# Performance work log

Hardware: AMD Instinct MI355X
Metric: run time of the kernel (lower is better)

The kernel has to match this reference:

```python
import jax, jax.numpy as jnp
import numpy as np

# Keyed conv layer as structured SpMM in affine coordinates.
# W (N x N sparse, N = C*H*W + 1) stored in ELL format: for each output row r,
# cols[r, :] are the K column indices and vals[r, :] the nonzero values.
C, H, W_, KS = 32, 32, 32, 3
N = C * H * W_ + 1          # 32769, homogeneous (+1 bias) dim
K = C * KS * KS             # 288 nnz per row (Toeplitz conv structure)
B = 32                      # batch


def setup_inputs() -> dict:
    key = jax.random.key(0)
    k1, k2, k3 = jax.random.split(key, 3)
    x_affine = jax.random.normal(k1, (B, N), dtype=jnp.float32)
    cols = jax.random.randint(k2, (N, K), 0, N, dtype=jnp.int32)
    vals = jax.random.normal(k3, (N, K), dtype=jnp.float32) / np.float32(np.sqrt(K))
    return {"x_affine": x_affine, "vals": vals, "cols": cols}


def reference(x_affine, vals, cols):
    # y = (W @ x_affine^T)^T  with W in row-wise ELL format.
    # Gather input features addressed by each row's nonzero columns, then
    # contract over the K nonzeros of each row.
    xg = x_affine[:, cols]                      # [B, N, K] gathered features
    y = jnp.einsum('bnk,nk->bn', xg, vals)      # [B, N]
    return y
```

## Files before the change

### kernel.cpp

```cpp
#include <hip/hip_runtime.h>

constexpr int B = 32;
constexpr int N = 32 * 32 * 32 + 1;
constexpr int K = 32 * 3 * 3;

using i4 = __attribute__((ext_vector_type(4))) int;
using f4 = __attribute__((ext_vector_type(4))) float;

__global__ __launch_bounds__(256) void transpose_x_kernel(
    const float* __restrict__ x, float* __restrict__ xT) {
  __shared__ float tile[32][33];
  const int n0 = blockIdx.x * 32;
  const int t  = threadIdx.x;
  const int lb = t & 31;
  const int lr = t >> 5;
#pragma unroll
  for (int i = 0; i < 4; ++i) {
    const int b = lr + i * 8;
    const int n = n0 + lb;
    float v = 0.f;
    if (n < N) v = x[(size_t)b * N + n];
    tile[lb][b] = v;
  }
  __syncthreads();
#pragma unroll
  for (int i = 0; i < 4; ++i) {
    const int nl = lr + i * 8;
    const int n  = n0 + nl;
    if (n < N) xT[(size_t)n * B + lb] = tile[nl][lb];
  }
}

__global__ __launch_bounds__(256) void gather_dot_lds_kernel(
    const float* __restrict__ xT, const float* __restrict__ vals,
    const int* __restrict__ cols, float* __restrict__ yT) {
  __shared__ int scols[32 * K];
  const int t    = threadIdx.x;
  const int lane = t & 63;
  const int wave = t >> 6;
  const int g    = lane >> 3;
  const int bq   = lane & 7;
  const int n0   = blockIdx.x * 32;

  constexpr int SLAB_BYTES = 32 * K * 4;
  constexpr int ROUNDS     = SLAB_BYTES / 4096;
  const char* slab = (const char*)(cols + (size_t)n0 * K);
  const long long avail = ((long long)N * K - (long long)n0 * K) * 4;
#pragma unroll
  for (int r = 0; r < ROUNDS; ++r) {
    const int off  = r * 4096 + t * 16;
    const int goff = (off + 16 <= avail) ? off : 0;
    __builtin_amdgcn_global_load_lds(
        (const __attribute__((address_space(1))) void*)(slab + goff),
        (__attribute__((address_space(3))) void*)((char*)scols + off),
        16, 0, 0);
  }
  __syncthreads();

  const int nl = wave * 8 + g;
  const int n  = n0 + nl;
  if (n >= N) return;

  const int*   __restrict__ srow = scols + nl * K;
  const float* __restrict__ vrow = vals + (size_t)n * K;

  f4 acc0 = {0.f, 0.f, 0.f, 0.f};
  f4 acc1 = {0.f, 0.f, 0.f, 0.f};

  const int rot = g * 8;

#pragma unroll 4
  for (int k = 0; k < K; k += 8) {
    int kk = k + rot;
    if (kk >= K) kk -= K;

    const i4 c0 = *reinterpret_cast<const i4*>(srow + kk);
    const i4 c1 = *reinterpret_cast<const i4*>(srow + kk + 4);
    const f4 v0 = *reinterpret_cast<const f4*>(vrow + kk);
    const f4 v1 = *reinterpret_cast<const f4*>(vrow + kk + 4);

    const f4 x0 = *reinterpret_cast<const f4*>(xT + (size_t)c0.x * B + bq * 4);
    const f4 x1 = *reinterpret_cast<const f4*>(xT + (size_t)c0.y * B + bq * 4);
    const f4 x2 = *reinterpret_cast<const f4*>(xT + (size_t)c0.z * B + bq * 4);
    const f4 x3 = *reinterpret_cast<const f4*>(xT + (size_t)c0.w * B + bq * 4);
    const f4 x4 = *reinterpret_cast<const f4*>(xT + (size_t)c1.x * B + bq * 4);
    const f4 x5 = *reinterpret_cast<const f4*>(xT + (size_t)c1.y * B + bq * 4);
    const f4 x6 = *reinterpret_cast<const f4*>(xT + (size_t)c1.z * B + bq * 4);
    const f4 x7 = *reinterpret_cast<const f4*>(xT + (size_t)c1.w * B + bq * 4);

    acc0 += x0 * v0.x;
    acc0 += x1 * v0.y;
    acc0 += x2 * v0.z;
    acc0 += x3 * v0.w;
    acc1 += x4 * v1.x;
    acc1 += x5 * v1.y;
    acc1 += x6 * v1.z;
    acc1 += x7 * v1.w;
  }

  acc0 += acc1;
  *reinterpret_cast<f4*>(yT + (size_t)n * B + bq * 4) = acc0;
}

__global__ __launch_bounds__(256) void transpose_y_kernel(
    const float* __restrict__ yT, float* __restrict__ y) {
  __shared__ float tile[32][33];
  const int n0 = blockIdx.x * 32;
  const int t  = threadIdx.x;
  const int lb = t & 31;
  const int lr = t >> 5;
#pragma unroll
  for (int i = 0; i < 4; ++i) {
    const int nl = lr + i * 8;
    const int n  = n0 + nl;
    float v = 0.f;
    if (n < N) v = yT[(size_t)n * B + lb];
    tile[nl][lb] = v;
  }
  __syncthreads();
#pragma unroll
  for (int i = 0; i < 4; ++i) {
    const int b = lr + i * 8;
    const int n = n0 + lb;
    if (n < N) y[(size_t)b * N + n] = tile[lb][b];
  }
}

__global__ __launch_bounds__(256) void gather_dot_fallback(
    const float* __restrict__ x, const float* __restrict__ vals,
    const int* __restrict__ cols, float* __restrict__ y) {
  const int t    = threadIdx.x;
  const int lane = t & 63;
  const int wave = t >> 6;
  const int g    = lane >> 3;
  const int bq   = lane & 7;
  const int n    = blockIdx.x * 32 + wave * 8 + g;
  if (n >= N) return;
  const int*   crow = cols + (size_t)n * K;
  const float* vrow = vals + (size_t)n * K;
  float4 acc = make_float4(0.f, 0.f, 0.f, 0.f);
  for (int k = 0; k < K; ++k) {
    const int   c = crow[k];
    const float v = vrow[k];
    acc.x += x[(size_t)(bq * 4 + 0) * N + c] * v;
    acc.y += x[(size_t)(bq * 4 + 1) * N + c] * v;
    acc.z += x[(size_t)(bq * 4 + 2) * N + c] * v;
    acc.w += x[(size_t)(bq * 4 + 3) * N + c] * v;
  }
  y[(size_t)(bq * 4 + 0) * N + n] = acc.x;
  y[(size_t)(bq * 4 + 1) * N + n] = acc.y;
  y[(size_t)(bq * 4 + 2) * N + n] = acc.z;
  y[(size_t)(bq * 4 + 3) * N + n] = acc.w;
}

extern "C" void kernel_launch(void* const* d_in, const int* in_sizes, int n_in,
                              void* d_out, int out_size, void* d_ws, size_t ws_size,
                              hipStream_t stream) {
  const float* x    = (const float*)d_in[0];
  const float* vals = (const float*)d_in[1];
  const int*   cols = (const int*)d_in[2];
  float*       y    = (float*)d_out;

  const size_t nb_elems = (size_t)N * B;
  const size_t need     = 2 * nb_elems * sizeof(float);

  const int nblocks = (N + 31) / 32;

  if (ws_size >= need) {
    float* xT = (float*)d_ws;
    float* yT = xT + nb_elems;
    transpose_x_kernel<<<nblocks, 256, 0, stream>>>(x, xT);
    gather_dot_lds_kernel<<<nblocks, 256, 0, stream>>>(xT, vals, cols, yT);
    transpose_y_kernel<<<nblocks, 256, 0, stream>>>(yT, y);
  } else {
    gather_dot_fallback<<<nblocks, 256, 0, stream>>>(x, vals, cols, y);
  }
}
```

Before: 176.2 us.

## Split K dimension across four blocks and stage vals in LDS

Splits the K reduction into four slices along grid.y, so each block stages only a quarter of its rows' cols and vals in LDS. This shrinks per-block LDS so more blocks can be resident, and it also stages vals through LDS. Partial sums go to four yT buffers via nontemporal stores and are summed in the output transpose kernel. The cost is three extra N*B partial buffers to write and read back, plus a larger workspace requirement.

```diff
diff --git a/kernel.cpp b/kernel.cpp
--- a/kernel.cpp
+++ b/kernel.cpp
@@ -3,6 +3,8 @@
 constexpr int B = 32;
 constexpr int N = 32 * 32 * 32 + 1;
 constexpr int K = 32 * 3 * 3;
+constexpr int KQ = K / 4;
+constexpr int NSPLIT = 4;
 
 using i4 = __attribute__((ext_vector_type(4))) int;
 using f4 = __attribute__((ext_vector_type(4))) float;
@@ -31,29 +33,54 @@
   }
 }
 
-__global__ __launch_bounds__(256) void gather_dot_lds_kernel(
+__global__ __launch_bounds__(256, 8) void gather_dot_q_kernel(
     const float* __restrict__ xT, const float* __restrict__ vals,
     const int* __restrict__ cols, float* __restrict__ yT) {
-  __shared__ int scols[32 * K];
+  __shared__ int   scols[32 * KQ];
+  __shared__ float svals[32 * KQ];
+
   const int t    = threadIdx.x;
   const int lane = t & 63;
   const int wave = t >> 6;
   const int g    = lane >> 3;
   const int bq   = lane & 7;
   const int n0   = blockIdx.x * 32;
-
-  constexpr int SLAB_BYTES = 32 * K * 4;
-  constexpr int ROUNDS     = SLAB_BYTES / 4096;
-  const char* slab = (const char*)(cols + (size_t)n0 * K);
-  const long long avail = ((long long)N * K - (long long)n0 * K) * 4;
-#pragma unroll
-  for (int r = 0; r < ROUNDS; ++r) {
-    const int off  = r * 4096 + t * 16;
-    const int goff = (off + 16 <= avail) ? off : 0;
-    __builtin_amdgcn_global_load_lds(
-        (const __attribute__((address_space(1))) void*)(slab + goff),
-        (__attribute__((address_space(3))) void*)((char*)scols + off),
-        16, 0, 0);
+  const int q    = blockIdx.y;
+  const int k0   = q * KQ;
+
+  {
+    const int nrow_clamp = N - 1;
+#pragma unroll
+    for (int r = 0; r < 2; ++r) {
+      const int c   = r * 256 + t;
+      const int row = c / 18;
+      const int off = c - row * 18;
+      const int nn  = (n0 + row <= nrow_clamp) ? (n0 + row) : nrow_clamp;
+      const size_t gi = (size_t)nn * K + k0 + off * 4;
+      __builtin_amdgcn_global_load_lds(
+          (const __attribute__((address_space(1))) void*)(cols + gi),
+          (__attribute__((address_space(3))) void*)((char*)scols + c * 16),
+          16, 0, 0);
+      __builtin_amdgcn_global_load_lds(
+          (const __attribute__((address_space(1))) void*)(vals + gi),
+          (__attribute__((address_space(3))) void*)((char*)svals + c * 16),
+          16, 0, 0);
+    }
+    if (t < 64) {
+      const int c   = 512 + t;
+      const int row = c / 18;
+      const int off = c - row * 18;
+      const int nn  = (n0 + row <= nrow_clamp) ? (n0 + row) : nrow_clamp;
+      const size_t gi = (size_t)nn * K + k0 + off * 4;
+      __builtin_amdgcn_global_load_lds(
+          (const __attribute__((address_space(1))) void*)(cols + gi),
+          (__attribute__((address_space(3))) void*)((char*)scols + c * 16),
+          16, 0, 0);
+      __builtin_amdgcn_global_load_lds(
+          (const __attribute__((address_space(1))) void*)(vals + gi),
+          (__attribute__((address_space(3))) void*)((char*)svals + c * 16),
+          16, 0, 0);
+    }
   }
   __syncthreads();
 
@@ -61,18 +88,18 @@
   const int n  = n0 + nl;
   if (n >= N) return;
 
-  const int*   __restrict__ srow = scols + nl * K;
-  const float* __restrict__ vrow = vals + (size_t)n * K;
+  const int*   __restrict__ srow = scols + nl * KQ;
+  const float* __restrict__ vrow = svals + nl * KQ;
 
   f4 acc0 = {0.f, 0.f, 0.f, 0.f};
   f4 acc1 = {0.f, 0.f, 0.f, 0.f};
 
   const int rot = g * 8;
 
-#pragma unroll 4
-  for (int k = 0; k < K; k += 8) {
+#pragma unroll 3
+  for (int k = 0; k < KQ; k += 8) {
     int kk = k + rot;
-    if (kk >= K) kk -= K;
+    if (kk >= KQ) kk -= KQ;
 
     const i4 c0 = *reinterpret_cast<const i4*>(srow + kk);
     const i4 c1 = *reinterpret_cast<const i4*>(srow + kk + 4);
@@ -99,22 +126,27 @@
   }
 
   acc0 += acc1;
-  *reinterpret_cast<f4*>(yT + (size_t)n * B + bq * 4) = acc0;
-}
-
-__global__ __launch_bounds__(256) void transpose_y_kernel(
+  __builtin_nontemporal_store(
+      acc0, reinterpret_cast<f4*>(yT + (size_t)q * N * B + (size_t)n * B + bq * 4));
+}
+
+__global__ __launch_bounds__(256) void transpose_y_sum4_kernel(
     const float* __restrict__ yT, float* __restrict__ y) {
   __shared__ float tile[32][33];
   const int n0 = blockIdx.x * 32;
   const int t  = threadIdx.x;
   const int lb = t & 31;
   const int lr = t >> 5;
+  constexpr size_t NB = (size_t)N * B;
 #pragma unroll
   for (int i = 0; i < 4; ++i) {
     const int nl = lr + i * 8;
     const int n  = n0 + nl;
     float v = 0.f;
-    if (n < N) v = yT[(size_t)n * B + lb];
+    if (n < N) {
+      const size_t idx = (size_t)n * B + lb;
+      v = yT[idx] + yT[NB + idx] + yT[2 * NB + idx] + yT[3 * NB + idx];
+    }
     tile[nl][lb] = v;
   }
   __syncthreads();
@@ -162,7 +194,7 @@
   float*       y    = (float*)d_out;
 
   const size_t nb_elems = (size_t)N * B;
-  const size_t need     = 2 * nb_elems * sizeof(float);
+  const size_t need = (1 + NSPLIT) * nb_elems * sizeof(float);
 
   const int nblocks = (N + 31) / 32;
 
@@ -170,8 +202,9 @@
     float* xT = (float*)d_ws;
     float* yT = xT + nb_elems;
     transpose_x_kernel<<<nblocks, 256, 0, stream>>>(x, xT);
-    gather_dot_lds_kernel<<<nblocks, 256, 0, stream>>>(xT, vals, cols, yT);
-    transpose_y_kernel<<<nblocks, 256, 0, stream>>>(yT, y);
+    dim3 grid(nblocks, NSPLIT);
+    gather_dot_q_kernel<<<grid, 256, 0, stream>>>(xT, vals, cols, yT);
+    transpose_y_sum4_kernel<<<nblocks, 256, 0, stream>>>(yT, y);
   } else {
     gather_dot_fallback<<<nblocks, 256, 0, stream>>>(x, vals, cols, y);
   }
```

Measured after the change: 193.5 us. 1.1x slower.
